# Optimization experiments

Hardware: AMD Instinct MI355X
Metric: run time of the kernel (lower is better)

Reference implementation:

```python
import jax, jax.numpy as jnp
import numpy as np
from jax import lax

IN_CHANNELS = 256
START_SIZE, STOP_SIZE, NUM_WINDOWS = 3, 65, 3
WINDOW_SIZES = np.linspace(START_SIZE, STOP_SIZE, NUM_WINDOWS).round().astype(int).tolist()  # [3, 34, 65]
EPS = 1e-12
NEG_SLOPE = 0.2


def setup_inputs() -> dict:
    key = jax.random.key(0)
    ks = jax.random.split(key, 9)
    N, C, H, W = 2, IN_CHANNELS, 128, 128
    feature = jax.random.normal(ks[0], (N, C, H, W), dtype=jnp.float32)
    c2 = 2 * C  # mean||std concat -> 512
    dims = [(c2, c2 // 2), (c2 // 2, 256), (256, 128), (128, 1)]
    Ws, bs = [], []
    for i, (din, dout) in enumerate(dims):
        Ws.append(jax.random.normal(ks[1 + i], (NUM_WINDOWS, dout, din), dtype=jnp.float32) / np.sqrt(din).astype(np.float32))
        bs.append(jnp.zeros((NUM_WINDOWS, dout), dtype=jnp.float32))
    return {"feature": feature,
            "W1": Ws[0], "b1": bs[0],
            "W2": Ws[1], "b2": bs[1],
            "W3": Ws[2], "b3": bs[2],
            "W4": Ws[3], "b4": bs[3],
            "label": 1}


def _window_stats(feature, K):
    # mean/std over K x K sliding windows, stride (K-1)//2, VALID padding.
    # Equivalent to F.unfold + var_mean(unbiased=False), but via windowed
    # sum / sum-of-squares accumulation (no O(K^2) blow-up).
    s = max(1, (K - 1) // 2)
    wd, ws = (1, 1, K, K), (1, 1, s, s)
    ssum = lax.reduce_window(feature, 0.0, lax.add, wd, ws, 'VALID')
    ssq = lax.reduce_window(feature * feature, 0.0, lax.add, wd, ws, 'VALID')
    n = jnp.float32(K * K)
    mean = ssum / n
    var = jnp.maximum(ssq / n - mean * mean, 0.0)
    std = jnp.sqrt(var + EPS)
    return jnp.concatenate([mean, std], axis=1)  # [N, 2C, NEW_H, NEW_W]


def _mlp(x, W1, b1, W2, b2, W3, b3, W4, b4):
    # x: [N, 2C]; 1x1 convs on a 1x1 spatial map == dense layers
    h = jax.nn.leaky_relu(x @ W1.T + b1, NEG_SLOPE)
    h = jax.nn.leaky_relu(h @ W2.T + b2, NEG_SLOPE)
    h = jax.nn.leaky_relu(h @ W3.T + b3, NEG_SLOPE)
    return h @ W4.T + b4  # [N, 1]


def reference(feature, W1, b1, W2, b2, W3, b3, W4, b4, label):
    y = jnp.float32(label)
    losses = jnp.float32(0.0)
    for i, K in enumerate(WINDOW_SIZES):
        stats = _window_stats(feature, K)          # [N, 2C, h, w]
        pooled = jnp.mean(stats, axis=(2, 3))      # [N, 2C]
        logits = _mlp(pooled, W1[i], b1[i], W2[i], b2[i], W3[i], b3[i], W4[i], b4[i])
        # BCE-with-logits vs constant target y: softplus(l) - l*y, averaged
        losses = losses + jnp.mean(jax.nn.softplus(logits) - logits * y)
    return losses
```

## Files before the change

### kernel.cpp

```cpp
#include <hip/hip_runtime.h>
#include <hip/hip_bf16.h>
#include <math.h>

#define CCH   256
#define HH    128
#define WW    128
#define EPSF  1e-12f
#define EPS81 8.1e-11f
#define SLOPE 0.2f


__device__ __forceinline__ void k3_loadrow(const float* __restrict__ plane, int r, int jb,
                                           float4& rs, float4& rq) {
    const float* rp = &plane[r * WW + jb];
    float4 v = *reinterpret_cast<const float4*>(rp);
    float2 w = *reinterpret_cast<const float2*>(rp + 4);
    float t12 = v.y + v.z, t34 = v.w + w.x;
    rs.x = v.x + t12; rs.y = t12 + v.w; rs.z = v.z + t34; rs.w = t34 + w.y;
    float y0 = v.x * v.x, y1 = v.y * v.y, y2 = v.z * v.z;
    float y3 = v.w * v.w, y4 = w.x * w.x, y5 = w.y * w.y;
    float u12 = y1 + y2, u34 = y3 + y4;
    rq.x = y0 + u12; rq.y = u12 + y3; rq.z = y2 + u34; rq.w = u34 + y5;
}

__device__ __forceinline__ void win_acc(float S, float Q, float wm, float& aS, float& aD) {
    float d = fmaxf(fmaf(S, -S, 9.f * Q), 0.f);
    aS = fmaf(wm, S, aS);
    aD = fmaf(wm, sqrtf(d + EPS81), aD);
}

__global__ __launch_bounds__(512, 4) void stats_kernel(const float* __restrict__ feat,
                                                       float* __restrict__ pooled,
                                                       int N) {
    __shared__ float plane[HH * WW + 8];
    __shared__ float wp[8][6];

    const int p    = blockIdx.x;
    const int n    = p >> 8;
    const int c    = p & 255;
    const int tid  = threadIdx.x;
    const int wave = tid >> 6, lane = tid & 63;

    {
        const float4* src4 = reinterpret_cast<const float4*>(feat + (size_t)p * (HH * WW));
        float4* pl4 = reinterpret_cast<float4*>(plane);
        #pragma unroll
        for (int i = 0; i < 8; ++i)
            pl4[tid + i * 512] = src4[tid + i * 512];
        if (tid < 8) plane[HH * WW + tid] = 0.f;
    }
    __syncthreads();

    float a3S = 0.f, a3D = 0.f;
    {
        const int s  = tid & 31;
        const int g  = tid >> 5;
        const int jb = s << 2;
        const float wm2 = (s < 31) ? 1.f : 0.f;
        const int i0 = g << 3;
        float4 r0s, r0q, r1s, r1q;
        k3_loadrow(plane, i0,     jb, r0s, r0q);
        k3_loadrow(plane, i0 + 1, jb, r1s, r1q);
        #pragma unroll 2
        for (int t = 0; t < 8; ++t) {
            int i = i0 + t;
            if (i < 126) {
                float4 r2s, r2q;
                k3_loadrow(plane, i + 2, jb, r2s, r2q);
                float Sx = r0s.x + r1s.x + r2s.x, Qx = r0q.x + r1q.x + r2q.x;
                float Sy = r0s.y + r1s.y + r2s.y, Qy = r0q.y + r1q.y + r2q.y;
                float Sz = r0s.z + r1s.z + r2s.z, Qz = r0q.z + r1q.z + r2q.z;
                float Sw = r0s.w + r1s.w + r2s.w, Qw = r0q.w + r1q.w + r2q.w;
                win_acc(Sx, Qx, 1.f, a3S, a3D);
                win_acc(Sy, Qy, 1.f, a3S, a3D);
                win_acc(Sz, Qz, wm2, a3S, a3D);
                win_acc(Sw, Qw, wm2, a3S, a3D);
                r0s = r1s; r0q = r1q; r1s = r2s; r1q = r2q;
            }
        }
    }

    float am34 = 0.f, as34 = 0.f;
    for (int w = wave; w < 36; w += 8) {
        int wi = w / 6, wj = w - 6 * wi;
        int r0 = wi << 4, c0 = wj << 4;
        float S = 0.f, Q = 0.f;
        #pragma unroll
        for (int it = 0; it < 5; ++it) {
            int t = lane + (it << 6);
            if (t < 306) {
                int r = t / 9, c4 = t - 9 * r;
                const float* rp = &plane[(r0 + r) * WW + c0 + (c4 << 2)];
                float4 v = *reinterpret_cast<const float4*>(rp);
                if (c4 == 8) { v.z = 0.f; v.w = 0.f; }
                S += (v.x + v.y) + (v.z + v.w);
                Q = fmaf(v.x, v.x, Q); Q = fmaf(v.y, v.y, Q);
                Q = fmaf(v.z, v.z, Q); Q = fmaf(v.w, v.w, Q);
            }
        }
        #pragma unroll
        for (int off = 32; off > 0; off >>= 1) {
            S += __shfl_down(S, off);
            Q += __shfl_down(Q, off);
        }
        if (lane == 0) {
            const float inv = 1.f / 1156.f;
            float mean = S * inv;
            float var  = fmaxf(fmaf(-mean, mean, Q * inv), 0.f);
            am34 += mean;
            as34 += sqrtf(var + EPSF);
        }
    }

    float m65 = 0.f, s65 = 0.f;
    if (wave >= 4) {
        int w  = wave - 4;
        int wi = w >> 1, wj = w & 1;
        int r0 = wi << 5, c0 = wj << 5;
        float S = 0.f, Q = 0.f;
        #pragma unroll
        for (int it = 0; it < 18; ++it) {
            int t = lane + (it << 6);
            if (t < 1105) {
                int r = t / 17, c4 = t - 17 * r;
                const float* rp = &plane[(r0 + r) * WW + c0 + (c4 << 2)];
                float4 v = *reinterpret_cast<const float4*>(rp);
                if (c4 == 16) { v.y = 0.f; v.z = 0.f; v.w = 0.f; }
                S += (v.x + v.y) + (v.z + v.w);
                Q = fmaf(v.x, v.x, Q); Q = fmaf(v.y, v.y, Q);
                Q = fmaf(v.z, v.z, Q); Q = fmaf(v.w, v.w, Q);
            }
        }
        #pragma unroll
        for (int off = 32; off > 0; off >>= 1) {
            S += __shfl_down(S, off);
            Q += __shfl_down(Q, off);
        }
        if (lane == 0) {
            const float inv = 1.f / 4225.f;
            float mean = S * inv;
            float var  = fmaxf(fmaf(-mean, mean, Q * inv), 0.f);
            m65 = mean;
            s65 = sqrtf(var + EPSF);
        }
    }

    #pragma unroll
    for (int off = 32; off > 0; off >>= 1) {
        a3S += __shfl_down(a3S, off);
        a3D += __shfl_down(a3D, off);
    }
    if (lane == 0) {
        wp[wave][0] = a3S; wp[wave][1] = a3D;
        wp[wave][2] = am34; wp[wave][3] = as34;
        wp[wave][4] = m65;  wp[wave][5] = s65;
    }
    __syncthreads();
    if (tid == 0) {
        float A3 = 0.f, D3 = 0.f, M34 = 0.f, S34 = 0.f, M65 = 0.f, S65 = 0.f;
        #pragma unroll
        for (int w = 0; w < 8; ++w) {
            A3 += wp[w][0]; D3 += wp[w][1];
            M34 += wp[w][2]; S34 += wp[w][3];
            M65 += wp[w][4]; S65 += wp[w][5];
        }
        const float inv3 = 1.f / (9.f * 126.f * 126.f);
        pooled[(0 * N + n) * 512 + c]       = A3 * inv3;
        pooled[(0 * N + n) * 512 + 256 + c] = D3 * inv3;
        pooled[(1 * N + n) * 512 + c]       = M34 * (1.f / 36.f);
        pooled[(1 * N + n) * 512 + 256 + c] = S34 * (1.f / 36.f);
        pooled[(2 * N + n) * 512 + c]       = M65 * 0.25f;
        pooled[(2 * N + n) * 512 + 256 + c] = S65 * 0.25f;
    }
}

__device__ __forceinline__ float leaky(float v) { return v > 0.f ? v : SLOPE * v; }

__global__ __launch_bounds__(256) void layer_kernel(const float* __restrict__ W,
                                                    const float* __restrict__ b,
                                                    const float* __restrict__ xin,
                                                    float* __restrict__ xout,
                                                    int DIN, int DOUT, int act) {
    const int wave = threadIdx.x >> 6, lane = threadIdx.x & 63;
    const int r = blockIdx.x * 4 + wave;
    if (r >= 3 * DOUT) return;
    const int k = r / DOUT, o = r - k * DOUT;
    const int DIN4 = DIN >> 2;

    const float4* w4  = reinterpret_cast<const float4*>(W + ((size_t)k * DOUT + o) * DIN);
    const float4* x04 = reinterpret_cast<const float4*>(xin + (size_t)(k * 2 + 0) * DIN);
    const float4* x14 = reinterpret_cast<const float4*>(xin + (size_t)(k * 2 + 1) * DIN);

    float s0 = 0.f, s1 = 0.f;
    for (int j = lane; j < DIN4; j += 64) {
        float4 wv = w4[j], a = x04[j], d = x14[j];
        s0 = fmaf(wv.x, a.x, s0); s0 = fmaf(wv.y, a.y, s0);
        s0 = fmaf(wv.z, a.z, s0); s0 = fmaf(wv.w, a.w, s0);
        s1 = fmaf(wv.x, d.x, s1); s1 = fmaf(wv.y, d.y, s1);
        s1 = fmaf(wv.z, d.z, s1); s1 = fmaf(wv.w, d.w, s1);
    }
    #pragma unroll
    for (int off = 32; off > 0; off >>= 1) {
        s0 += __shfl_down(s0, off);
        s1 += __shfl_down(s1, off);
    }
    if (lane == 0) {
        float bb = b[k * DOUT + o];
        float v0 = s0 + bb, v1 = s1 + bb;
        if (act) { v0 = leaky(v0); v1 = leaky(v1); }
        xout[(size_t)(k * 2 + 0) * DOUT + o] = v0;
        xout[(size_t)(k * 2 + 1) * DOUT + o] = v1;
    }
}

__global__ __launch_bounds__(384) void final_kernel(const float* __restrict__ W4,
                                                    const float* __restrict__ b4,
                                                    const float* __restrict__ h3,
                                                    const int* __restrict__ label,
                                                    float* __restrict__ out, int N) {
    __shared__ float lossArr[8];
    const int wave = threadIdx.x >> 6, lane = threadIdx.x & 63;
    if (wave < 3 * N) {
        const int k = wave / N, n = wave - k * N;
        const float* w = &W4[(size_t)k * 128];
        const float* x = &h3[(size_t)(k * N + n) * 128];
        float s = w[lane] * x[lane] + w[lane + 64] * x[lane + 64];
        #pragma unroll
        for (int off = 32; off > 0; off >>= 1) s += __shfl_down(s, off);
        if (lane == 0) {
            float logit = s + b4[k];
            float y = (float)(*label);
            float sp = fmaxf(logit, 0.f) + log1pf(expf(-fabsf(logit)));
            lossArr[wave] = sp - logit * y;
        }
    }
    __syncthreads();
    if (threadIdx.x == 0) {
        float tot = 0.f;
        for (int k = 0; k < 3; ++k) {
            float s = 0.f;
            for (int nn = 0; nn < N; ++nn) s += lossArr[k * N + nn];
            tot += s / (float)N;
        }
        out[0] = tot;
    }
}

extern "C" void kernel_launch(void* const* d_in, const int* in_sizes, int n_in,
                              void* d_out, int out_size, void* d_ws, size_t ws_size,
                              hipStream_t stream) {
    const float* feat = (const float*)d_in[0];
    const float* W1   = (const float*)d_in[1];
    const float* b1   = (const float*)d_in[2];
    const float* W2   = (const float*)d_in[3];
    const float* b2   = (const float*)d_in[4];
    const float* W3   = (const float*)d_in[5];
    const float* b3   = (const float*)d_in[6];
    const float* W4   = (const float*)d_in[7];
    const float* b4   = (const float*)d_in[8];
    const int* label  = (const int*)d_in[9];

    const int N = in_sizes[0] / (CCH * HH * WW);

    float* pooled = (float*)d_ws;
    float* h1     = pooled + (size_t)3 * N * 512;
    float* h2     = h1     + (size_t)3 * N * 256;
    float* h3     = h2     + (size_t)3 * N * 256;

    stats_kernel<<<N * CCH, 512, 0, stream>>>(feat, pooled, N);

    layer_kernel<<<192, 256, 0, stream>>>(W1, b1, pooled, h1, 512, 256, 1);
    layer_kernel<<<192, 256, 0, stream>>>(W2, b2, h1, h2, 256, 256, 1);
    layer_kernel<<<96, 256, 0, stream>>>(W3, b3, h2, h3, 256, 128, 1);
    final_kernel<<<1, 384, 0, stream>>>(W4, b4, h3, label, (float*)d_out, N);
}
```

Before: 32.62 us.

## Fuse MLP layers into one kernel, use global_load_lds staging, unroll K3 loop

Replaces the four chained MLP launches with one fused kernel per (window, batch) pair that keeps activations in shared memory, plus a tiny finalize kernel. This cuts the launch count from five to three. The stats kernel now copies the feature plane into LDS with the direct global-to-LDS load builtin instead of going through registers. The K=3 row loop is fully unrolled, with the bounds branch replaced by zero weights and a clamped row index. The fused MLP runs on only six blocks, so each block reads its weights with little parallelism, and the finalize kernel hardcodes N=2.

```diff
diff --git a/kernel.cpp b/kernel.cpp
--- a/kernel.cpp
+++ b/kernel.cpp
@@ -42,11 +42,14 @@
     const int wave = tid >> 6, lane = tid & 63;
 
     {
-        const float4* src4 = reinterpret_cast<const float4*>(feat + (size_t)p * (HH * WW));
-        float4* pl4 = reinterpret_cast<float4*>(plane);
-        #pragma unroll
-        for (int i = 0; i < 8; ++i)
-            pl4[tid + i * 512] = src4[tid + i * 512];
+        const float* gbase = feat + (size_t)p * (HH * WW) + (tid << 2);
+        #pragma unroll
+        for (int i = 0; i < 8; ++i) {
+            __builtin_amdgcn_global_load_lds(
+                (const __attribute__((address_space(1))) void*)(gbase + i * 2048),
+                (__attribute__((address_space(3))) void*)&plane[i * 2048 + (wave << 8)],
+                16, 0, 0);
+        }
         if (tid < 8) plane[HH * WW + tid] = 0.f;
     }
     __syncthreads();
@@ -61,22 +64,23 @@
         float4 r0s, r0q, r1s, r1q;
         k3_loadrow(plane, i0,     jb, r0s, r0q);
         k3_loadrow(plane, i0 + 1, jb, r1s, r1q);
-        #pragma unroll 2
+        #pragma unroll
         for (int t = 0; t < 8; ++t) {
-            int i = i0 + t;
-            if (i < 126) {
-                float4 r2s, r2q;
-                k3_loadrow(plane, i + 2, jb, r2s, r2q);
-                float Sx = r0s.x + r1s.x + r2s.x, Qx = r0q.x + r1q.x + r2q.x;
-                float Sy = r0s.y + r1s.y + r2s.y, Qy = r0q.y + r1q.y + r2q.y;
-                float Sz = r0s.z + r1s.z + r2s.z, Qz = r0q.z + r1q.z + r2q.z;
-                float Sw = r0s.w + r1s.w + r2s.w, Qw = r0q.w + r1q.w + r2q.w;
-                win_acc(Sx, Qx, 1.f, a3S, a3D);
-                win_acc(Sy, Qy, 1.f, a3S, a3D);
-                win_acc(Sz, Qz, wm2, a3S, a3D);
-                win_acc(Sw, Qw, wm2, a3S, a3D);
-                r0s = r1s; r0q = r1q; r1s = r2s; r1q = r2q;
-            }
+            const int i  = i0 + t;
+            const int r2 = (i + 2 < 128) ? (i + 2) : 127;
+            float4 r2s, r2q;
+            k3_loadrow(plane, r2, jb, r2s, r2q);
+            const float wr  = (i < 126) ? 1.f : 0.f;
+            const float wrm = wr * wm2;
+            float Sx = r0s.x + r1s.x + r2s.x, Qx = r0q.x + r1q.x + r2q.x;
+            float Sy = r0s.y + r1s.y + r2s.y, Qy = r0q.y + r1q.y + r2q.y;
+            float Sz = r0s.z + r1s.z + r2s.z, Qz = r0q.z + r1q.z + r2q.z;
+            float Sw = r0s.w + r1s.w + r2s.w, Qw = r0q.w + r1q.w + r2q.w;
+            win_acc(Sx, Qx, wr,  a3S, a3D);
+            win_acc(Sy, Qy, wr,  a3S, a3D);
+            win_acc(Sz, Qz, wrm, a3S, a3D);
+            win_acc(Sw, Qw, wrm, a3S, a3D);
+            r0s = r1s; r0q = r1q; r1s = r2s; r1q = r2q;
         }
     }
 
@@ -176,72 +180,107 @@
 
 __device__ __forceinline__ float leaky(float v) { return v > 0.f ? v : SLOPE * v; }
 
-__global__ __launch_bounds__(256) void layer_kernel(const float* __restrict__ W,
-                                                    const float* __restrict__ b,
-                                                    const float* __restrict__ xin,
-                                                    float* __restrict__ xout,
-                                                    int DIN, int DOUT, int act) {
-    const int wave = threadIdx.x >> 6, lane = threadIdx.x & 63;
-    const int r = blockIdx.x * 4 + wave;
-    if (r >= 3 * DOUT) return;
-    const int k = r / DOUT, o = r - k * DOUT;
-    const int DIN4 = DIN >> 2;
-
-    const float4* w4  = reinterpret_cast<const float4*>(W + ((size_t)k * DOUT + o) * DIN);
-    const float4* x04 = reinterpret_cast<const float4*>(xin + (size_t)(k * 2 + 0) * DIN);
-    const float4* x14 = reinterpret_cast<const float4*>(xin + (size_t)(k * 2 + 1) * DIN);
-
-    float s0 = 0.f, s1 = 0.f;
-    for (int j = lane; j < DIN4; j += 64) {
-        float4 wv = w4[j], a = x04[j], d = x14[j];
-        s0 = fmaf(wv.x, a.x, s0); s0 = fmaf(wv.y, a.y, s0);
-        s0 = fmaf(wv.z, a.z, s0); s0 = fmaf(wv.w, a.w, s0);
-        s1 = fmaf(wv.x, d.x, s1); s1 = fmaf(wv.y, d.y, s1);
-        s1 = fmaf(wv.z, d.z, s1); s1 = fmaf(wv.w, d.w, s1);
-    }
-    #pragma unroll
-    for (int off = 32; off > 0; off >>= 1) {
-        s0 += __shfl_down(s0, off);
-        s1 += __shfl_down(s1, off);
-    }
-    if (lane == 0) {
-        float bb = b[k * DOUT + o];
-        float v0 = s0 + bb, v1 = s1 + bb;
-        if (act) { v0 = leaky(v0); v1 = leaky(v1); }
-        xout[(size_t)(k * 2 + 0) * DOUT + o] = v0;
-        xout[(size_t)(k * 2 + 1) * DOUT + o] = v1;
-    }
-}
-
-__global__ __launch_bounds__(384) void final_kernel(const float* __restrict__ W4,
-                                                    const float* __restrict__ b4,
-                                                    const float* __restrict__ h3,
-                                                    const int* __restrict__ label,
-                                                    float* __restrict__ out, int N) {
-    __shared__ float lossArr[8];
-    const int wave = threadIdx.x >> 6, lane = threadIdx.x & 63;
-    if (wave < 3 * N) {
-        const int k = wave / N, n = wave - k * N;
-        const float* w = &W4[(size_t)k * 128];
-        const float* x = &h3[(size_t)(k * N + n) * 128];
-        float s = w[lane] * x[lane] + w[lane + 64] * x[lane + 64];
+__global__ __launch_bounds__(1024) void mlp_fused(const float* __restrict__ pooled,
+                                                  const float* __restrict__ W1, const float* __restrict__ b1,
+                                                  const float* __restrict__ W2, const float* __restrict__ b2,
+                                                  const float* __restrict__ W3, const float* __restrict__ b3,
+                                                  const float* __restrict__ W4, const float* __restrict__ b4,
+                                                  const int* __restrict__ label,
+                                                  float* __restrict__ losses) {
+    __shared__ float x[512];
+    __shared__ float h1[256];
+    __shared__ float h2[256];
+    __shared__ float h3[128];
+
+    const int bk = blockIdx.x;
+    const int k  = bk >> 1;
+    const int tid = threadIdx.x;
+    const int wave = tid >> 6, lane = tid & 63;
+
+    if (tid < 128)
+        reinterpret_cast<float4*>(x)[tid] =
+            reinterpret_cast<const float4*>(pooled + (size_t)bk * 512)[tid];
+    __syncthreads();
+
+    {
+        const float4* x4 = reinterpret_cast<const float4*>(x);
+        #pragma unroll 2
+        for (int rr = 0; rr < 16; ++rr) {
+            int o = (wave << 4) + rr;
+            const float4* w4 = reinterpret_cast<const float4*>(W1 + ((size_t)k * 256 + o) * 512);
+            float4 wa = w4[lane], wb = w4[lane + 64];
+            float4 xa = x4[lane], xb = x4[lane + 64];
+            float s = 0.f;
+            s = fmaf(wa.x, xa.x, s); s = fmaf(wa.y, xa.y, s);
+            s = fmaf(wa.z, xa.z, s); s = fmaf(wa.w, xa.w, s);
+            s = fmaf(wb.x, xb.x, s); s = fmaf(wb.y, xb.y, s);
+            s = fmaf(wb.z, xb.z, s); s = fmaf(wb.w, xb.w, s);
+            #pragma unroll
+            for (int off = 32; off > 0; off >>= 1) s += __shfl_down(s, off);
+            if (lane == 0) h1[o] = leaky(s + b1[k * 256 + o]);
+        }
+    }
+    __syncthreads();
+
+    {
+        const float4* h14 = reinterpret_cast<const float4*>(h1);
+        #pragma unroll 2
+        for (int rr = 0; rr < 16; ++rr) {
+            int o = (wave << 4) + rr;
+            const float4* w4 = reinterpret_cast<const float4*>(W2 + ((size_t)k * 256 + o) * 256);
+            float4 wa = w4[lane], xa = h14[lane];
+            float s = 0.f;
+            s = fmaf(wa.x, xa.x, s); s = fmaf(wa.y, xa.y, s);
+            s = fmaf(wa.z, xa.z, s); s = fmaf(wa.w, xa.w, s);
+            #pragma unroll
+            for (int off = 32; off > 0; off >>= 1) s += __shfl_down(s, off);
+            if (lane == 0) h2[o] = leaky(s + b2[k * 256 + o]);
+        }
+    }
+    __syncthreads();
+
+    {
+        const float4* h24 = reinterpret_cast<const float4*>(h2);
+        #pragma unroll 2
+        for (int rr = 0; rr < 8; ++rr) {
+            int o = (wave << 3) + rr;
+            const float4* w4 = reinterpret_cast<const float4*>(W3 + ((size_t)k * 128 + o) * 256);
+            float4 wa = w4[lane], xa = h24[lane];
+            float s = 0.f;
+            s = fmaf(wa.x, xa.x, s); s = fmaf(wa.y, xa.y, s);
+            s = fmaf(wa.z, xa.z, s); s = fmaf(wa.w, xa.w, s);
+            #pragma unroll
+            for (int off = 32; off > 0; off >>= 1) s += __shfl_down(s, off);
+            if (lane == 0) h3[o] = leaky(s + b3[k * 128 + o]);
+        }
+    }
+    __syncthreads();
+
+    if (wave == 0) {
+        float s = 0.f;
+        if (lane < 32) {
+            float4 wv = reinterpret_cast<const float4*>(W4 + (size_t)k * 128)[lane];
+            float4 hv = reinterpret_cast<const float4*>(h3)[lane];
+            s = fmaf(wv.x, hv.x, s); s = fmaf(wv.y, hv.y, s);
+            s = fmaf(wv.z, hv.z, s); s = fmaf(wv.w, hv.w, s);
+        }
         #pragma unroll
         for (int off = 32; off > 0; off >>= 1) s += __shfl_down(s, off);
         if (lane == 0) {
             float logit = s + b4[k];
             float y = (float)(*label);
             float sp = fmaxf(logit, 0.f) + log1pf(expf(-fabsf(logit)));
-            lossArr[wave] = sp - logit * y;
-        }
-    }
-    __syncthreads();
-    if (threadIdx.x == 0) {
+            losses[bk] = sp - logit * y;
+        }
+    }
+}
+
+__global__ void finalize_kernel(const float* __restrict__ losses, float* __restrict__ out) {
+    if (threadIdx.x == 0 && blockIdx.x == 0) {
         float tot = 0.f;
-        for (int k = 0; k < 3; ++k) {
-            float s = 0.f;
-            for (int nn = 0; nn < N; ++nn) s += lossArr[k * N + nn];
-            tot += s / (float)N;
-        }
+        #pragma unroll
+        for (int k = 0; k < 3; ++k)
+            tot += (losses[k * 2 + 0] + losses[k * 2 + 1]) / 2.f;
         out[0] = tot;
     }
 }
@@ -263,14 +302,10 @@
     const int N = in_sizes[0] / (CCH * HH * WW);
 
     float* pooled = (float*)d_ws;
-    float* h1     = pooled + (size_t)3 * N * 512;
-    float* h2     = h1     + (size_t)3 * N * 256;
-    float* h3     = h2     + (size_t)3 * N * 256;
+    float* losses = pooled + (size_t)3 * N * 512;
 
     stats_kernel<<<N * CCH, 512, 0, stream>>>(feat, pooled, N);
-
-    layer_kernel<<<192, 256, 0, stream>>>(W1, b1, pooled, h1, 512, 256, 1);
-    layer_kernel<<<192, 256, 0, stream>>>(W2, b2, h1, h2, 256, 256, 1);
-    layer_kernel<<<96, 256, 0, stream>>>(W3, b3, h2, h3, 256, 128, 1);
-    final_kernel<<<1, 384, 0, stream>>>(W4, b4, h3, label, (float*)d_out, N);
-}
+    mlp_fused<<<3 * N, 1024, 0, stream>>>(pooled, W1, b1, W2, b2, W3, b3, W4, b4,
+                                          label, losses);
+    finalize_kernel<<<1, 64, 0, stream>>>(losses, (float*)d_out);
+}
```

Measured after the change: 58.48 us. 79.3% more time.
